# Optimization experiments

Hardware: AMD Instinct MI355X
Metric: run time of the kernel (lower is better)

The kernel has to match this reference:

```python
import jax, jax.numpy as jnp
import numpy as np

# Dims
B, S, D, N, K, NOPS = 4, 2048, 512, 16, 4, 4
NUM_LAYERS = 1
SCALE = 1.0 / float(np.sqrt(NUM_LAYERS))   # base_layer.residual_scale
GAMMA = 0.01                                # lindblad_gamma
COND_THRESH = 100.0                         # condition_threshold
MHC_ITERS, MHC_TAU = 10, 0.05


def setup_inputs() -> dict:
    key = jax.random.key(0)
    ks = jax.random.split(key, 16)
    def rn(k, shape, s=0.02):
        return jax.random.normal(k, shape, dtype=jnp.float32) * s
    return {
        "x_real": jax.random.normal(ks[0], (B, S, D), dtype=jnp.float32),
        "x_imag": jax.random.normal(ks[1], (B, S, D), dtype=jnp.float32),
        "Win_r": rn(ks[2], (D, D)), "Win_i": rn(ks[3], (D, D)),
        "conv_w": rn(ks[4], (K, D), 0.5),
        "W_dt": rn(ks[5], (D, D)), "b_dt": jnp.full((D,), -4.0, jnp.float32),
        "A_log": jnp.tile(jnp.log(jnp.arange(1, N + 1, dtype=jnp.float32)), (D, 1)),
        "W_B": rn(ks[6], (D, N)), "W_C": rn(ks[7], (D, N)),
        "D_skip": jnp.ones((D,), jnp.float32),
        "Wout_r": rn(ks[8], (D, D)), "Wout_i": rn(ks[9], (D, D)),
        "L_r": rn(ks[10], (NOPS, D), 0.1), "L_i": rn(ks[11], (NOPS, D), 0.1),
        "phi": rn(ks[12], (D,), 0.1),
        "H_res_logits": jnp.zeros((1, 1), jnp.float32),
        "H_res_logits_imag": jnp.zeros((1, 1), jnp.float32),
    }


def _causal_dwconv(u, w):
    # u: [B,S,D] complex, w: [K,D] real depthwise causal kernel
    Kk, Ss = w.shape[0], u.shape[1]
    up = jnp.pad(u, ((0, 0), (Kk - 1, 0), (0, 0)))
    return sum(w[k][None, None, :] * up[:, k:k + Ss, :] for k in range(Kk))


def _forward(x_real, x_imag, Win_r, Win_i, conv_w, W_dt, b_dt, A_log, W_B, W_C,
             D_skip, Wout_r, Wout_i, L_r, L_i, phi, H_res_logits, H_res_logits_imag):
    x = jax.lax.complex(x_real, x_imag)                       # [B,S,D] complex64
    # ---- base ComplexMamba3Layer: complex in-proj -> causal dwconv -> mod-gate -> selective scan -> out-proj ----
    u = x @ jax.lax.complex(Win_r, Win_i)
    u = _causal_dwconv(u, conv_w)
    u = u * jax.nn.sigmoid(jnp.abs(u)).astype(u.dtype)        # magnitude gate (modSiLU)
    xr = u.real
    dt = jax.nn.softplus(xr @ W_dt + b_dt)                    # [B,S,D]
    Bm = xr @ W_B                                             # [B,S,N]
    Cm = xr @ W_C                                             # [B,S,N]
    A = -jnp.exp(A_log)                                       # [D,N]
    def step(h, inp):
        dt_t, Bm_t, Cm_t, u_t = inp                            # [B,D],[B,N],[B,N],[B,D]c
        decay = jnp.exp(dt_t[..., None] * A).astype(h.dtype)  # [B,D,N]
        h = decay * h + (dt_t.astype(u_t.dtype) * u_t)[..., None] * Bm_t[:, None, :].astype(u_t.dtype)
        y_t = jnp.einsum('bdn,bn->bd', h, Cm_t.astype(h.dtype))
        return h, y_t
    h0 = jnp.zeros((x.shape[0], D, N), dtype=u.dtype)
    xs = (jnp.swapaxes(dt, 0, 1), jnp.swapaxes(Bm, 0, 1), jnp.swapaxes(Cm, 0, 1), jnp.swapaxes(u, 0, 1))
    _, ys = jax.lax.scan(step, h0, xs)
    y = jnp.swapaxes(ys, 0, 1) + D_skip.astype(u.dtype) * u
    y = y @ jax.lax.complex(Wout_r, Wout_i)
    out = x + SCALE * y
    # ---- V8 wrapper ----
    branch = (out - x) / max(SCALE, 1e-8)
    # Lindblad dissipation: psi * (1 - gamma * sum_k |L_k|^2), diagonal jump operators
    coeff = jnp.sum(L_r ** 2 + L_i ** 2, axis=0)              # [D]
    branch = branch * (1.0 - GAMMA * coeff).astype(branch.dtype)
    # approximate Hamiltonian (no-grad): H = (1/S) sum_s |psi_s><psi_s|
    mag = jnp.abs(branch)
    H = jax.lax.stop_gradient(jnp.einsum('bsd,bse->bde', mag, mag) / mag.shape[1])
    # hybrid automata: _H_prev is None on the first forward -> no jump applied (faithful to source)
    # quaternionic escape: condition proxy from H diagonal, phase rotation if singular
    diag = jnp.diagonal(H, axis1=1, axis2=2)                  # [B,D]
    cond = jnp.max(diag, axis=-1) / (jnp.min(diag, axis=-1) + 1e-8)
    escaped = cond > COND_THRESH                              # [B]
    rot = jnp.exp(jax.lax.complex(jnp.zeros_like(phi), phi))  # unit phase per dim
    branch = jnp.where(escaped[:, None, None], branch * rot, branch)
    branch = branch * SCALE
    # mHC residual: Sinkhorn on 1x1 logits (streams=1) with complex phase
    M = jnp.exp(H_res_logits / MHC_TAU)
    for _ in range(MHC_ITERS):
        M = M / jnp.sum(M, axis=1, keepdims=True)
        M = M / jnp.sum(M, axis=0, keepdims=True)
    coef = M[0, 0] * jnp.exp(jax.lax.complex(jnp.zeros(()), H_res_logits_imag[0, 0]))
    out = x + coef.astype(branch.dtype) * branch
    return jnp.stack([out.real, out.imag])                    # [2,B,S,D] real view


def reference(x_real, x_imag, Win_r, Win_i, conv_w, W_dt, b_dt, A_log, W_B, W_C,
              D_skip, Wout_r, Wout_i, L_r, L_i, phi, H_res_logits, H_res_logits_imag):
    return _forward(x_real, x_imag, Win_r, Win_i, conv_w, W_dt, b_dt, A_log, W_B, W_C,
                    D_skip, Wout_r, Wout_i, L_r, L_i, phi, H_res_logits, H_res_logits_imag)
```

## Files before the change

kernel.cpp:

```cpp
#include <hip/hip_runtime.h>
#include <math.h>

#define BB 4
#define SSEQ 2048
#define DDIM 512
#define NSTATE 16
#define KCONV 4
#define NOPS_ 4
#define GAMMA_ 0.01f
#define CONDT_ 100.0f
#define SCALE_ 1.0f
#define NC 64
#define LC 32
#define NCOLF 576

static const size_t BSD = (size_t)BB * SSEQ * DDIM;
static const size_t BSN = (size_t)BB * SSEQ * NSTATE;
static const size_t MIDSZ = (size_t)BB * NC * DDIM * NSTATE;

typedef short short8v __attribute__((ext_vector_type(8)));
typedef float f32x4 __attribute__((ext_vector_type(4)));

__device__ __forceinline__ short f2bf(float x) {
    union { float f; unsigned int u; } v; v.f = x;
    unsigned int u = v.u + 0x7FFFu + ((v.u >> 16) & 1u);
    return (short)(u >> 16);
}
__device__ __forceinline__ short8v cvt8(const float4 a, const float4 b) {
    short8v r;
    r[0] = f2bf(a.x); r[1] = f2bf(a.y); r[2] = f2bf(a.z); r[3] = f2bf(a.w);
    r[4] = f2bf(b.x); r[5] = f2bf(b.y); r[6] = f2bf(b.z); r[7] = f2bf(b.w);
    return r;
}

__global__ __launch_bounds__(256) void convert_weights(
    const float* __restrict__ W0, const float* __restrict__ W1,
    const float* __restrict__ W2, const float* __restrict__ W3,
    const float* __restrict__ W4,
    unsigned short* __restrict__ T0, unsigned short* __restrict__ T1,
    unsigned short* __restrict__ T2, unsigned short* __restrict__ T3,
    unsigned short* __restrict__ T4)
{
    __shared__ float tile[64][65];
    const int n0 = (blockIdx.x & 7) * 64, k0 = (blockIdx.x >> 3) * 64;
    const float* srcs[5] = {W0, W1, W2, W3, W4};
    unsigned short* dsts[5] = {T0, T1, T2, T3, T4};
    #pragma unroll
    for (int m = 0; m < 5; ++m) {
        const float* W = srcs[m];
        unsigned short* T = dsts[m];
        for (int it = 0; it < 16; ++it) {
            const int idx = it * 256 + threadIdx.x;
            const int r = idx >> 6, c = idx & 63;
            tile[r][c] = W[(size_t)(k0 + r) * DDIM + n0 + c];
        }
        __syncthreads();
        for (int it = 0; it < 16; ++it) {
            const int idx = it * 256 + threadIdx.x;
            const int r = idx >> 6, c = idx & 63;
            T[(size_t)(n0 + r) * DDIM + k0 + c] = (unsigned short)f2bf(tile[c][r]);
        }
        __syncthreads();
    }
}

__global__ __launch_bounds__(256) void convert_bc(
    const float* __restrict__ WB, const float* __restrict__ WC,
    unsigned short* __restrict__ WdtT)
{
    const int idx = blockIdx.x * 256 + threadIdx.x;
    const int r = idx >> 9;
    const int k = idx & 511;
    float v = 0.f;
    if (r < 16) v = WB[(size_t)k * NSTATE + r];
    else if (r < 32) v = WC[(size_t)k * NSTATE + (r - 16)];
    WdtT[(size_t)(512 + r) * DDIM + k] = (unsigned short)f2bf(v);
}

template <bool LIND>
__global__ __launch_bounds__(256, 4) void cgemm_mfma(
    const float* __restrict__ Ar, const float* __restrict__ Ai,
    const unsigned short* __restrict__ WTr, const unsigned short* __restrict__ WTi,
    const float* __restrict__ Lr, const float* __restrict__ Li,
    float* __restrict__ Cr, float* __restrict__ Ci)
{
    __shared__ unsigned short Ar_s[64 * 32], Ai_s[64 * 32];
    __shared__ unsigned short Br_s[64 * 32], Bi_s[64 * 32];
    const int tid = threadIdx.x;
    const int lane = tid & 63, wave = tid >> 6;
    const int wm = wave >> 1, wn = wave & 1;
    const int col0 = blockIdx.x * 64;
    const int row0 = blockIdx.y * 64;
    const int srow = tid >> 2;
    const int q = tid & 3;

    f32x4 accr[2][2], acci[2][2];
    #pragma unroll
    for (int a = 0; a < 2; ++a)
        #pragma unroll
        for (int b = 0; b < 2; ++b) { accr[a][b] = (f32x4)0.f; acci[a][b] = (f32x4)0.f; }

    for (int k0 = 0; k0 < DDIM; k0 += 32) {
        {
            const size_t ab = (size_t)(row0 + srow) * DDIM + k0 + q * 8;
            const float4 r0 = *reinterpret_cast<const float4*>(Ar + ab);
            const float4 r1 = *reinterpret_cast<const float4*>(Ar + ab + 4);
            const float4 i0 = *reinterpret_cast<const float4*>(Ai + ab);
            const float4 i1 = *reinterpret_cast<const float4*>(Ai + ab + 4);
            const int ix = srow * 32 + ((q ^ ((srow >> 1) & 3)) << 3);
            *reinterpret_cast<short8v*>(&Ar_s[ix]) = cvt8(r0, r1);
            *reinterpret_cast<short8v*>(&Ai_s[ix]) = cvt8(i0, i1);
            const size_t wb = (size_t)(col0 + srow) * DDIM + k0 + q * 8;
            *reinterpret_cast<short8v*>(&Br_s[ix]) = *reinterpret_cast<const short8v*>(WTr + wb);
            *reinterpret_cast<short8v*>(&Bi_s[ix]) = *reinterpret_cast<const short8v*>(WTi + wb);
        }
        __syncthreads();
        short8v ar[2], ai[2], ain[2], wr[2], wi[2];
        const int ks = lane >> 4;
        #pragma unroll
        for (int mi = 0; mi < 2; ++mi) {
            const int r = wm * 32 + mi * 16 + (lane & 15);
            const int idx = r * 32 + ((ks ^ ((r >> 1) & 3)) << 3);
            ar[mi] = *reinterpret_cast<const short8v*>(&Ar_s[idx]);
            ai[mi] = *reinterpret_cast<const short8v*>(&Ai_s[idx]);
            #pragma unroll
            for (int j = 0; j < 8; ++j) ain[mi][j] = ai[mi][j] ^ (short)0x8000;
        }
        #pragma unroll
        for (int nj = 0; nj < 2; ++nj) {
            const int n = wn * 32 + nj * 16 + (lane & 15);
            const int idx = n * 32 + ((ks ^ ((n >> 1) & 3)) << 3);
            wr[nj] = *reinterpret_cast<const short8v*>(&Br_s[idx]);
            wi[nj] = *reinterpret_cast<const short8v*>(&Bi_s[idx]);
        }
        #pragma unroll
        for (int mi = 0; mi < 2; ++mi)
            #pragma unroll
            for (int nj = 0; nj < 2; ++nj) {
                accr[mi][nj] = __builtin_amdgcn_mfma_f32_16x16x32_bf16(ar[mi], wr[nj], accr[mi][nj], 0, 0, 0);
                accr[mi][nj] = __builtin_amdgcn_mfma_f32_16x16x32_bf16(ain[mi], wi[nj], accr[mi][nj], 0, 0, 0);
                acci[mi][nj] = __builtin_amdgcn_mfma_f32_16x16x32_bf16(ar[mi], wi[nj], acci[mi][nj], 0, 0, 0);
                acci[mi][nj] = __builtin_amdgcn_mfma_f32_16x16x32_bf16(ai[mi], wr[nj], acci[mi][nj], 0, 0, 0);
            }
        __syncthreads();
    }
    float lindv[2] = {1.f, 1.f};
    if (LIND) {
        #pragma unroll
        for (int nj = 0; nj < 2; ++nj) {
            const int col = col0 + wn * 32 + nj * 16 + (lane & 15);
            float s = 0.f;
            #pragma unroll
            for (int k = 0; k < NOPS_; ++k) {
                const float lr = Lr[k * DDIM + col], li = Li[k * DDIM + col];
                s += lr * lr + li * li;
            }
            lindv[nj] = 1.0f - GAMMA_ * s;
        }
    }
    #pragma unroll
    for (int mi = 0; mi < 2; ++mi)
        #pragma unroll
        for (int nj = 0; nj < 2; ++nj) {
            const int col = col0 + wn * 32 + nj * 16 + (lane & 15);
            #pragma unroll
            for (int rr = 0; rr < 4; ++rr) {
                const int row = row0 + wm * 32 + mi * 16 + (lane >> 4) * 4 + rr;
                Cr[(size_t)row * DDIM + col] = accr[mi][nj][rr] * lindv[nj];
                Ci[(size_t)row * DDIM + col] = acci[mi][nj][rr] * lindv[nj];
            }
        }
}

__global__ __launch_bounds__(256, 4) void rgemm_fused(
    const float* __restrict__ A, const unsigned short* __restrict__ WT,
    const float* __restrict__ bias, float* __restrict__ Out,
    float* __restrict__ Bm, float* __restrict__ Cm)
{
    __shared__ unsigned short A_s[64 * 32], B_s[64 * 32];
    const int tid = threadIdx.x;
    const int lane = tid & 63, wave = tid >> 6;
    const int wm = wave >> 1, wn = wave & 1;
    const int col0 = blockIdx.x * 64;
    const int row0 = blockIdx.y * 64;
    const int srow = tid >> 2, q = tid & 3;

    f32x4 acc[2][2];
    #pragma unroll
    for (int a = 0; a < 2; ++a)
        #pragma unroll
        for (int b = 0; b < 2; ++b) acc[a][b] = (f32x4)0.f;

    for (int k0 = 0; k0 < DDIM; k0 += 32) {
        {
            const size_t ab = (size_t)(row0 + srow) * DDIM + k0 + q * 8;
            const float4 r0 = *reinterpret_cast<const float4*>(A + ab);
            const float4 r1 = *reinterpret_cast<const float4*>(A + ab + 4);
            const int ix = srow * 32 + ((q ^ ((srow >> 1) & 3)) << 3);
            *reinterpret_cast<short8v*>(&A_s[ix]) = cvt8(r0, r1);
            const size_t wb = (size_t)(col0 + srow) * DDIM + k0 + q * 8;
            *reinterpret_cast<short8v*>(&B_s[ix]) = *reinterpret_cast<const short8v*>(WT + wb);
        }
        __syncthreads();
        short8v av[2], bv[2];
        const int ks = lane >> 4;
        #pragma unroll
        for (int mi = 0; mi < 2; ++mi) {
            const int r = wm * 32 + mi * 16 + (lane & 15);
            av[mi] = *reinterpret_cast<const short8v*>(&A_s[r * 32 + ((ks ^ ((r >> 1) & 3)) << 3)]);
        }
        #pragma unroll
        for (int nj = 0; nj < 2; ++nj) {
            const int n = wn * 32 + nj * 16 + (lane & 15);
            bv[nj] = *reinterpret_cast<const short8v*>(&B_s[n * 32 + ((ks ^ ((n >> 1) & 3)) << 3)]);
        }
        #pragma unroll
        for (int mi = 0; mi < 2; ++mi)
            #pragma unroll
            for (int nj = 0; nj < 2; ++nj)
                acc[mi][nj] = __builtin_amdgcn_mfma_f32_16x16x32_bf16(av[mi], bv[nj], acc[mi][nj], 0, 0, 0);
        __syncthreads();
    }
    #pragma unroll
    for (int mi = 0; mi < 2; ++mi)
        #pragma unroll
        for (int nj = 0; nj < 2; ++nj) {
            const int col = col0 + wn * 32 + nj * 16 + (lane & 15);
            if (col < 512) {
                const float bz = bias[col];
                #pragma unroll
                for (int rr = 0; rr < 4; ++rr) {
                    const int row = row0 + wm * 32 + mi * 16 + (lane >> 4) * 4 + rr;
                    const float z = acc[mi][nj][rr] + bz;
                    Out[(size_t)row * DDIM + col] = (z > 0.f) ? (z + log1pf(expf(-z))) : log1pf(expf(z));
                }
            } else if (col < 528) {
                #pragma unroll
                for (int rr = 0; rr < 4; ++rr) {
                    const int row = row0 + wm * 32 + mi * 16 + (lane >> 4) * 4 + rr;
                    Bm[(size_t)row * NSTATE + (col - 512)] = acc[mi][nj][rr];
                }
            } else if (col < 544) {
                #pragma unroll
                for (int rr = 0; rr < 4; ++rr) {
                    const int row = row0 + wm * 32 + mi * 16 + (lane >> 4) * 4 + rr;
                    Cm[(size_t)row * NSTATE + (col - 528)] = acc[mi][nj][rr];
                }
            }
        }
}

__global__ __launch_bounds__(256) void conv_gate_kernel(
    const float* __restrict__ ur, const float* __restrict__ ui,
    const float* __restrict__ w, float* __restrict__ gr, float* __restrict__ gi)
{
    const size_t idx = (size_t)blockIdx.x * 256 + threadIdx.x;
    const int d = (int)(idx % DDIM);
    const int s = (int)((idx / DDIM) % SSEQ);
    float ar = 0.f, ai = 0.f;
    #pragma unroll
    for (int k = 0; k < KCONV; ++k) {
        const int soff = s + k - (KCONV - 1);
        if (soff >= 0) {
            const size_t j = idx + (size_t)((long)(k - (KCONV - 1)) * DDIM);
            const float wk = w[k * DDIM + d];
            ar += wk * ur[j];
            ai += wk * ui[j];
        }
    }
    const float mag = sqrtf(ar * ar + ai * ai);
    const float sig = 1.0f / (1.0f + expf(-mag));
    gr[idx] = ar * sig;
    gi[idx] = ai * sig;
}

__global__ __launch_bounds__(256) void scan_phase1(
    const float* __restrict__ dt, const float* __restrict__ gr, const float* __restrict__ gi,
    const float* __restrict__ Bm, const float* __restrict__ A_log,
    float* __restrict__ mid_hr, float* __restrict__ mid_hi, float* __restrict__ dtsum)
{
    __shared__ float bm_s[LC * NSTATE];
    const int blk = blockIdx.x;
    const int dblk = blk & 1;
    const int c = (blk >> 1) & (NC - 1);
    const int b = blk >> 7;
    const int tid = threadIdx.x;
    const int d = dblk * 256 + tid;
    const int s0 = c * LC;
    {
        const size_t base = ((size_t)b * SSEQ + s0) * NSTATE;
        bm_s[tid] = Bm[base + tid];
        bm_s[tid + 256] = Bm[base + tid + 256];
    }
    float A_dn[16], hr[16], hi[16];
    #pragma unroll
    for (int n = 0; n < 16; ++n) {
        A_dn[n] = -expf(A_log[d * NSTATE + n]);
        hr[n] = 0.f; hi[n] = 0.f;
    }
    float dts = 0.f;
    __syncthreads();
    const size_t gbase = (size_t)b * SSEQ * DDIM + (size_t)s0 * DDIM + d;
    for (int i = 0; i < LC; ++i) {
        const float dtv = dt[gbase + (size_t)i * DDIM];
        const float ur = gr[gbase + (size_t)i * DDIM];
        const float ui = gi[gbase + (size_t)i * DDIM];
        dts += dtv;
        const float xr = dtv * ur, xi = dtv * ui;
        #pragma unroll
        for (int n = 0; n < 16; ++n) {
            const float a = expf(dtv * A_dn[n]);
            const float bmv = bm_s[i * 16 + n];
            hr[n] = a * hr[n] + xr * bmv;
            hi[n] = a * hi[n] + xi * bmv;
        }
    }
    const size_t mbase = ((size_t)(b * NC + c) * DDIM + d) * NSTATE;
    #pragma unroll
    for (int n = 0; n < 16; ++n) { mid_hr[mbase + n] = hr[n]; mid_hi[mbase + n] = hi[n]; }
    dtsum[(size_t)(b * NC + c) * DDIM + d] = dts;
}

__global__ __launch_bounds__(256) void scan_phase2(
    const float* __restrict__ mid_hr, const float* __restrict__ mid_hi,
    const float* __restrict__ dtsum, const float* __restrict__ A_log,
    float* __restrict__ hinit_r, float* __restrict__ hinit_i)
{
    const int gid = blockIdx.x * 256 + threadIdx.x;
    const int n = gid & 15;
    const int d = (gid >> 4) & (DDIM - 1);
    const int b = gid >> 13;
    const float A_dn = -expf(A_log[d * NSTATE + n]);
    float hr = 0.f, hi = 0.f;
    for (int c = 0; c < NC; ++c) {
        const size_t cb = (size_t)(b * NC + c) * DDIM + d;
        hinit_r[cb * NSTATE + n] = hr;
        hinit_i[cb * NSTATE + n] = hi;
        const float P = expf(A_dn * dtsum[cb]);
        hr = mid_hr[cb * NSTATE + n] + P * hr;
        hi = mid_hi[cb * NSTATE + n] + P * hi;
    }
}

__global__ __launch_bounds__(256) void scan_phase3(
    const float* __restrict__ dt, const float* __restrict__ gr, const float* __restrict__ gi,
    const float* __restrict__ Bm, const float* __restrict__ Cm,
    const float* __restrict__ A_log, const float* __restrict__ D_skip,
    const float* __restrict__ hinit_r, const float* __restrict__ hinit_i,
    float* __restrict__ yr, float* __restrict__ yi)
{
    __shared__ float bm_s[LC * NSTATE], cm_s[LC * NSTATE];
    const int blk = blockIdx.x;
    const int dblk = blk & 1;
    const int c = (blk >> 1) & (NC - 1);
    const int b = blk >> 7;
    const int tid = threadIdx.x;
    const int d = dblk * 256 + tid;
    const int s0 = c * LC;
    {
        const size_t base = ((size_t)b * SSEQ + s0) * NSTATE;
        bm_s[tid] = Bm[base + tid];
        bm_s[tid + 256] = Bm[base + tid + 256];
        cm_s[tid] = Cm[base + tid];
        cm_s[tid + 256] = Cm[base + tid + 256];
    }
    float A_dn[16], hr[16], hi[16];
    const size_t mbase = ((size_t)(b * NC + c) * DDIM + d) * NSTATE;
    #pragma unroll
    for (int n = 0; n < 16; ++n) {
        A_dn[n] = -expf(A_log[d * NSTATE + n]);
        hr[n] = hinit_r[mbase + n];
        hi[n] = hinit_i[mbase + n];
    }
    const float dsk = D_skip[d];
    __syncthreads();
    const size_t gbase = (size_t)b * SSEQ * DDIM + (size_t)s0 * DDIM + d;
    for (int i = 0; i < LC; ++i) {
        const float dtv = dt[gbase + (size_t)i * DDIM];
        const float ur = gr[gbase + (size_t)i * DDIM];
        const float ui = gi[gbase + (size_t)i * DDIM];
        const float xr = dtv * ur, xi = dtv * ui;
        float accr = dsk * ur, acci = dsk * ui;
        #pragma unroll
        for (int n = 0; n < 16; ++n) {
            const float a = expf(dtv * A_dn[n]);
            const float bmv = bm_s[i * 16 + n], cmv = cm_s[i * 16 + n];
            hr[n] = a * hr[n] + xr * bmv;
            hi[n] = a * hi[n] + xi * bmv;
            accr += hr[n] * cmv;
            acci += hi[n] * cmv;
        }
        yr[gbase + (size_t)i * DDIM] = accr;
        yi[gbase + (size_t)i * DDIM] = acci;
    }
}

__global__ __launch_bounds__(256) void diag_kernel(
    const float* __restrict__ br, const float* __restrict__ bi, float* __restrict__ diag)
{
    const int b = blockIdx.x >> 4;
    const int s0 = (blockIdx.x & 15) * 128;
    const int t = threadIdx.x;
    float a0 = 0.f, a1 = 0.f;
    for (int i = 0; i < 128; ++i) {
        const size_t g = (size_t)b * SSEQ * DDIM + (size_t)(s0 + i) * DDIM;
        const float r0 = br[g + t], i0 = bi[g + t];
        const float r1 = br[g + t + 256], i1 = bi[g + t + 256];
        a0 += r0 * r0 + i0 * i0;
        a1 += r1 * r1 + i1 * i1;
    }
    const float inv = 1.0f / (float)SSEQ;
    atomicAdd(&diag[b * DDIM + t], a0 * inv);
    atomicAdd(&diag[b * DDIM + t + 256], a1 * inv);
}

__global__ __launch_bounds__(256) void escape_kernel(
    const float* __restrict__ diag, const float* __restrict__ phi,
    const float* __restrict__ logit, const float* __restrict__ logit_im,
    float* __restrict__ misc, float* __restrict__ rot_r, float* __restrict__ rot_i)
{
    const int tid = threadIdx.x;
    rot_r[tid] = cosf(phi[tid]);
    rot_i[tid] = sinf(phi[tid]);
    rot_r[tid + 256] = cosf(phi[tid + 256]);
    rot_i[tid + 256] = sinf(phi[tid + 256]);
    const int b = tid >> 6, lane = tid & 63;
    float mx = -1e30f, mn = 1e30f;
    for (int j = lane; j < DDIM; j += 64) {
        const float v = diag[b * DDIM + j];
        mx = fmaxf(mx, v);
        mn = fminf(mn, v);
    }
    #pragma unroll
    for (int off = 32; off; off >>= 1) {
        mx = fmaxf(mx, __shfl_xor(mx, off));
        mn = fminf(mn, __shfl_xor(mn, off));
    }
    if (lane == 0) {
        const float cond = mx / (mn + 1e-8f);
        misc[b] = (cond > CONDT_) ? 1.0f : 0.0f;
    }
    if (tid == 0) {
        float M = expf(logit[0] / 0.05f);
        for (int it = 0; it < 10; ++it) { M = M / M; M = M / M; }
        const float im = logit_im[0];
        misc[4] = M * cosf(im);
        misc[5] = M * sinf(im);
    }
}

__global__ __launch_bounds__(256) void final_kernel(
    const float* __restrict__ xr, const float* __restrict__ xi,
    const float* __restrict__ br, const float* __restrict__ bi,
    const float* __restrict__ misc, const float* __restrict__ rot_r,
    const float* __restrict__ rot_i, float* __restrict__ out)
{
    const size_t idx = (size_t)blockIdx.x * 256 + threadIdx.x;
    const int d = (int)(idx % DDIM);
    const int b = (int)(idx / ((size_t)SSEQ * DDIM));
    float r = br[idx], im = bi[idx];
    if (misc[b] != 0.0f) {
        const float rr = rot_r[d], ri = rot_i[d];
        const float nr = r * rr - im * ri;
        const float ni = r * ri + im * rr;
        r = nr;
        im = ni;
    }
    r *= SCALE_;
    im *= SCALE_;
    const float cr = misc[4], ci = misc[5];
    const float outr = r * cr - im * ci;
    const float outi = im * cr + r * ci;
    out[idx] = xr[idx] + outr;
    out[BSD + idx] = xi[idx] + outi;
}

extern "C" void kernel_launch(void* const* d_in, const int* in_sizes, int n_in,
                              void* d_out, int out_size, void* d_ws, size_t ws_size,
                              hipStream_t stream)
{
    (void)in_sizes; (void)n_in; (void)out_size; (void)ws_size;
    const float* x_r    = (const float*)d_in[0];
    const float* x_i    = (const float*)d_in[1];
    const float* Win_r  = (const float*)d_in[2];
    const float* Win_i  = (const float*)d_in[3];
    const float* convw  = (const float*)d_in[4];
    const float* W_dt   = (const float*)d_in[5];
    const float* b_dt   = (const float*)d_in[6];
    const float* A_log  = (const float*)d_in[7];
    const float* W_B    = (const float*)d_in[8];
    const float* W_C    = (const float*)d_in[9];
    const float* D_skip = (const float*)d_in[10];
    const float* Wout_r = (const float*)d_in[11];
    const float* Wout_i = (const float*)d_in[12];
    const float* L_r    = (const float*)d_in[13];
    const float* L_i    = (const float*)d_in[14];
    const float* phi    = (const float*)d_in[15];
    const float* hres   = (const float*)d_in[16];
    const float* hresi  = (const float*)d_in[17];
    float* out = (float*)d_out;

    float* f    = (float*)d_ws;
    float* u_r  = f;
    float* u_i  = f + BSD;
    float* g_r  = f + 2 * BSD;
    float* g_i  = f + 3 * BSD;
    float* dt   = f + 4 * BSD;
    float* y_r  = f + 5 * BSD;
    float* y_i  = f + 6 * BSD;
    float* Bm   = f + 7 * BSD;
    float* Cm   = Bm + BSN;
    float* dtsum = Cm + BSN;
    float* diag = dtsum + (size_t)BB * NC * DDIM;
    float* misc = diag + (size_t)BB * DDIM;
    float* rot_r = misc + 8;
    float* rot_i = rot_r + DDIM;
    unsigned short* wbase = (unsigned short*)(rot_i + DDIM);
    unsigned short* WinT_r  = wbase;
    unsigned short* WinT_i  = wbase + 1 * 262144;
    unsigned short* WoutT_r = wbase + 2 * 262144;
    unsigned short* WoutT_i = wbase + 3 * 262144;
    unsigned short* WdtT    = wbase + 4 * 262144;
    float* mid_hr  = u_r;
    float* mid_hi  = u_r + MIDSZ;
    float* hinit_r = u_i;
    float* hinit_i = u_i + MIDSZ;
    float* br_r = u_r;
    float* br_i = u_i;

    convert_weights<<<64, 256, 0, stream>>>(Win_r, Win_i, Wout_r, Wout_i, W_dt,
                                            WinT_r, WinT_i, WoutT_r, WoutT_i, WdtT);
    convert_bc<<<128, 256, 0, stream>>>(W_B, W_C, WdtT);
    cgemm_mfma<false><<<dim3(8, 128), 256, 0, stream>>>(
        x_r, x_i, WinT_r, WinT_i, nullptr, nullptr, u_r, u_i);
    conv_gate_kernel<<<(int)(BSD / 256), 256, 0, stream>>>(u_r, u_i, convw, g_r, g_i);
    rgemm_fused<<<dim3(9, 128), 256, 0, stream>>>(g_r, WdtT, b_dt, dt, Bm, Cm);
    scan_phase1<<<BB * NC * 2, 256, 0, stream>>>(dt, g_r, g_i, Bm, A_log, mid_hr, mid_hi, dtsum);
    scan_phase2<<<128, 256, 0, stream>>>(mid_hr, mid_hi, dtsum, A_log, hinit_r, hinit_i);
    scan_phase3<<<BB * NC * 2, 256, 0, stream>>>(dt, g_r, g_i, Bm, Cm, A_log, D_skip,
                                                 hinit_r, hinit_i, y_r, y_i);
    cgemm_mfma<true><<<dim3(8, 128), 256, 0, stream>>>(
        y_r, y_i, WoutT_r, WoutT_i, L_r, L_i, br_r, br_i);
    hipMemsetAsync(diag, 0, (size_t)BB * DDIM * sizeof(float), stream);
    diag_kernel<<<64, 256, 0, stream>>>(br_r, br_i, diag);
    escape_kernel<<<1, 256, 0, stream>>>(diag, phi, hres, hresi, misc, rot_r, rot_i);
    final_kernel<<<(int)(BSD / 256), 256, 0, stream>>>(
        x_r, x_i, br_r, br_i, misc, rot_r, rot_i, out);
}
```

Baseline: 413.9 us.

## Halve scan chunk length, use fast exp intrinsics, and reuse scan buffers in place

Splits the chunked selective scan into 128 chunks of 16 steps instead of 64 of 32. This doubles the block count of the two heavy scan phases and shortens their serial loops, at the cost of a longer serial carry pass in phase 2. Phase 2 now overwrites the per-chunk partial states in place with the chunk initial states, which removes the separate hinit buffers. Precise expf/log1pf calls in the gate, softplus and scan are replaced by __expf/__logf intrinsics, trading some accuracy for fewer instructions. The diag reduction kernel is spread over 4x more blocks with shorter loops.

```diff
diff --git a/kernel.cpp b/kernel.cpp
--- a/kernel.cpp
+++ b/kernel.cpp
@@ -10,9 +10,8 @@
 #define GAMMA_ 0.01f
 #define CONDT_ 100.0f
 #define SCALE_ 1.0f
-#define NC 64
-#define LC 32
-#define NCOLF 576
+#define NC 128
+#define LC 16
 
 static const size_t BSD = (size_t)BB * SSEQ * DDIM;
 static const size_t BSN = (size_t)BB * SSEQ * NSTATE;
@@ -232,7 +231,8 @@
                 for (int rr = 0; rr < 4; ++rr) {
                     const int row = row0 + wm * 32 + mi * 16 + (lane >> 4) * 4 + rr;
                     const float z = acc[mi][nj][rr] + bz;
-                    Out[(size_t)row * DDIM + col] = (z > 0.f) ? (z + log1pf(expf(-z))) : log1pf(expf(z));
+                    Out[(size_t)row * DDIM + col] =
+                        (z > 0.f) ? (z + __logf(1.f + __expf(-z))) : __logf(1.f + __expf(z));
                 }
             } else if (col < 528) {
                 #pragma unroll
@@ -269,7 +269,7 @@
         }
     }
     const float mag = sqrtf(ar * ar + ai * ai);
-    const float sig = 1.0f / (1.0f + expf(-mag));
+    const float sig = 1.0f / (1.0f + __expf(-mag));
     gr[idx] = ar * sig;
     gi[idx] = ai * sig;
 }
@@ -283,19 +283,15 @@
     const int blk = blockIdx.x;
     const int dblk = blk & 1;
     const int c = (blk >> 1) & (NC - 1);
-    const int b = blk >> 7;
+    const int b = blk >> 8;
     const int tid = threadIdx.x;
     const int d = dblk * 256 + tid;
     const int s0 = c * LC;
-    {
-        const size_t base = ((size_t)b * SSEQ + s0) * NSTATE;
-        bm_s[tid] = Bm[base + tid];
-        bm_s[tid + 256] = Bm[base + tid + 256];
-    }
+    bm_s[tid] = Bm[((size_t)b * SSEQ + s0) * NSTATE + tid];
     float A_dn[16], hr[16], hi[16];
     #pragma unroll
     for (int n = 0; n < 16; ++n) {
-        A_dn[n] = -expf(A_log[d * NSTATE + n]);
+        A_dn[n] = -__expf(A_log[d * NSTATE + n]);
         hr[n] = 0.f; hi[n] = 0.f;
     }
     float dts = 0.f;
@@ -309,7 +305,7 @@
         const float xr = dtv * ur, xi = dtv * ui;
         #pragma unroll
         for (int n = 0; n < 16; ++n) {
-            const float a = expf(dtv * A_dn[n]);
+            const float a = __expf(dtv * A_dn[n]);
             const float bmv = bm_s[i * 16 + n];
             hr[n] = a * hr[n] + xr * bmv;
             hi[n] = a * hi[n] + xi * bmv;
@@ -322,23 +318,24 @@
 }
 
 __global__ __launch_bounds__(256) void scan_phase2(
-    const float* __restrict__ mid_hr, const float* __restrict__ mid_hi,
-    const float* __restrict__ dtsum, const float* __restrict__ A_log,
-    float* __restrict__ hinit_r, float* __restrict__ hinit_i)
+    float* __restrict__ mid_hr, float* __restrict__ mid_hi,
+    const float* __restrict__ dtsum, const float* __restrict__ A_log)
 {
     const int gid = blockIdx.x * 256 + threadIdx.x;
     const int n = gid & 15;
     const int d = (gid >> 4) & (DDIM - 1);
     const int b = gid >> 13;
-    const float A_dn = -expf(A_log[d * NSTATE + n]);
+    const float A_dn = -__expf(A_log[d * NSTATE + n]);
     float hr = 0.f, hi = 0.f;
     for (int c = 0; c < NC; ++c) {
         const size_t cb = (size_t)(b * NC + c) * DDIM + d;
-        hinit_r[cb * NSTATE + n] = hr;
-        hinit_i[cb * NSTATE + n] = hi;
-        const float P = expf(A_dn * dtsum[cb]);
-        hr = mid_hr[cb * NSTATE + n] + P * hr;
-        hi = mid_hi[cb * NSTATE + n] + P * hi;
+        const float mr = mid_hr[cb * NSTATE + n];
+        const float mi = mid_hi[cb * NSTATE + n];
+        mid_hr[cb * NSTATE + n] = hr;
+        mid_hi[cb * NSTATE + n] = hi;
+        const float P = __expf(A_dn * dtsum[cb]);
+        hr = mr + P * hr;
+        hi = mi + P * hi;
     }
 }
 
@@ -353,22 +350,20 @@
     const int blk = blockIdx.x;
     const int dblk = blk & 1;
     const int c = (blk >> 1) & (NC - 1);
-    const int b = blk >> 7;
+    const int b = blk >> 8;
     const int tid = threadIdx.x;
     const int d = dblk * 256 + tid;
     const int s0 = c * LC;
     {
         const size_t base = ((size_t)b * SSEQ + s0) * NSTATE;
         bm_s[tid] = Bm[base + tid];
-        bm_s[tid + 256] = Bm[base + tid + 256];
         cm_s[tid] = Cm[base + tid];
-        cm_s[tid + 256] = Cm[base + tid + 256];
     }
     float A_dn[16], hr[16], hi[16];
     const size_t mbase = ((size_t)(b * NC + c) * DDIM + d) * NSTATE;
     #pragma unroll
     for (int n = 0; n < 16; ++n) {
-        A_dn[n] = -expf(A_log[d * NSTATE + n]);
+        A_dn[n] = -__expf(A_log[d * NSTATE + n]);
         hr[n] = hinit_r[mbase + n];
         hi[n] = hinit_i[mbase + n];
     }
@@ -383,7 +378,7 @@
         float accr = dsk * ur, acci = dsk * ui;
         #pragma unroll
         for (int n = 0; n < 16; ++n) {
-            const float a = expf(dtv * A_dn[n]);
+            const float a = __expf(dtv * A_dn[n]);
             const float bmv = bm_s[i * 16 + n], cmv = cm_s[i * 16 + n];
             hr[n] = a * hr[n] + xr * bmv;
             hi[n] = a * hi[n] + xi * bmv;
@@ -398,11 +393,11 @@
 __global__ __launch_bounds__(256) void diag_kernel(
     const float* __restrict__ br, const float* __restrict__ bi, float* __restrict__ diag)
 {
-    const int b = blockIdx.x >> 4;
-    const int s0 = (blockIdx.x & 15) * 128;
+    const int b = blockIdx.x >> 6;
+    const int s0 = (blockIdx.x & 63) * 32;
     const int t = threadIdx.x;
     float a0 = 0.f, a1 = 0.f;
-    for (int i = 0; i < 128; ++i) {
+    for (int i = 0; i < 32; ++i) {
         const size_t g = (size_t)b * SSEQ * DDIM + (size_t)(s0 + i) * DDIM;
         const float r0 = br[g + t], i0 = bi[g + t];
         const float r1 = br[g + t + 256], i1 = bi[g + t + 256];
@@ -522,9 +517,7 @@
     unsigned short* WoutT_i = wbase + 3 * 262144;
     unsigned short* WdtT    = wbase + 4 * 262144;
     float* mid_hr  = u_r;
-    float* mid_hi  = u_r + MIDSZ;
-    float* hinit_r = u_i;
-    float* hinit_i = u_i + MIDSZ;
+    float* mid_hi  = u_i;
     float* br_r = u_r;
     float* br_i = u_i;
 
@@ -536,13 +529,13 @@
     conv_gate_kernel<<<(int)(BSD / 256), 256, 0, stream>>>(u_r, u_i, convw, g_r, g_i);
     rgemm_fused<<<dim3(9, 128), 256, 0, stream>>>(g_r, WdtT, b_dt, dt, Bm, Cm);
     scan_phase1<<<BB * NC * 2, 256, 0, stream>>>(dt, g_r, g_i, Bm, A_log, mid_hr, mid_hi, dtsum);
-    scan_phase2<<<128, 256, 0, stream>>>(mid_hr, mid_hi, dtsum, A_log, hinit_r, hinit_i);
+    scan_phase2<<<128, 256, 0, stream>>>(mid_hr, mid_hi, dtsum, A_log);
     scan_phase3<<<BB * NC * 2, 256, 0, stream>>>(dt, g_r, g_i, Bm, Cm, A_log, D_skip,
-                                                 hinit_r, hinit_i, y_r, y_i);
+                                                 mid_hr, mid_hi, y_r, y_i);
     cgemm_mfma<true><<<dim3(8, 128), 256, 0, stream>>>(
         y_r, y_i, WoutT_r, WoutT_i, L_r, L_i, br_r, br_i);
     hipMemsetAsync(diag, 0, (size_t)BB * DDIM * sizeof(float), stream);
-    diag_kernel<<<64, 256, 0, stream>>>(br_r, br_i, diag);
+    diag_kernel<<<256, 256, 0, stream>>>(br_r, br_i, diag);
     escape_kernel<<<1, 256, 0, stream>>>(diag, phi, hres, hresi, misc, rot_r, rot_i);
     final_kernel<<<(int)(BSD / 256), 256, 0, stream>>>(
         x_r, x_i, br_r, br_i, misc, rot_r, rot_i, out);
```

After: 362.7 us. -12.4%, faster.
